# Performance work log

Hardware: AMD Instinct MI355X
Metric: run time of the kernel (lower is better)

Reference implementation:

```python
import jax, jax.numpy as jnp
import numpy as np

N, E, IN, H = 10000, 320000, 128, 64

def setup_inputs() -> dict:
    key = jax.random.key(0)
    ks = jax.random.split(key, 6)
    x = jax.random.normal(ks[0], (N, IN), dtype=jnp.float32)
    edge_index = jax.random.randint(ks[1], (2, E), 0, N)
    edge_weight = jax.random.uniform(ks[2], (E,), dtype=jnp.float32)
    W_rel = jax.random.normal(ks[3], (IN, H), dtype=jnp.float32) / np.float32(np.sqrt(IN))
    W_root = jax.random.normal(ks[4], (IN, H), dtype=jnp.float32) / np.float32(np.sqrt(IN))
    b = jnp.zeros((H,), dtype=jnp.float32)
    return {"x": x, "edge_index": edge_index, "edge_weight": edge_weight,
            "W_rel": W_rel, "W_root": W_root, "b": b}

def reference(x, edge_index, edge_weight, W_rel, W_root, b):
    # GraphConv (PyG): out_i = W_rel @ sum_{j->i} e_ji * x_j + W_root @ x_i + b
    src, dst = edge_index[0], edge_index[1]
    msgs = x[src] * edge_weight[:, None]                    # [E, IN] gather
    agg = jax.ops.segment_sum(msgs, dst, num_segments=N)    # [N, IN] scatter-add
    z = agg @ W_rel + x @ W_root + b                        # [N, H]
    # (activation=None, dropout inactive in eval, no BN)
    adj = jax.nn.sigmoid(z @ z.T)                           # [N, N] inner-product decoder
    return adj, z
```

## Files before the change

kernel.cpp:

```cpp
#include <hip/hip_runtime.h>
#include <hip/hip_bf16.h>
#include <stdint.h>

#define N_NODES 10000
#define N_EDGES 320000
#define DIM_IN  128
#define DIM_H   64
#define SSTR    72

typedef __attribute__((ext_vector_type(8))) short  short8;
typedef __attribute__((ext_vector_type(4))) float  f32x4;

__device__ __forceinline__ unsigned short f2bf(float f) {
    union { float f; unsigned int i; } v; v.f = f;
    unsigned int u = v.i;
    return (unsigned short)((u + 0x7fffu + ((u >> 16) & 1u)) >> 16);
}

__global__ void hist_kernel(const int* __restrict__ ei, int* __restrict__ deg) {
    int e = blockIdx.x * blockDim.x + threadIdx.x;
    if (e < N_EDGES) atomicAdd(&deg[ei[N_EDGES + e]], 1);
}

__global__ void __launch_bounds__(1024) scan_kernel(const int* __restrict__ deg,
                                                    int* __restrict__ offs,
                                                    int* __restrict__ cursor) {
    __shared__ int part[1024];
    int t = threadIdx.x;
    int base = t * 10;
    int local[10];
    int s = 0;
    for (int i = 0; i < 10; ++i) {
        int idx = base + i;
        int d = (idx < N_NODES) ? deg[idx] : 0;
        local[i] = d; s += d;
    }
    part[t] = s;
    __syncthreads();
    for (int o = 1; o < 1024; o <<= 1) {
        int add = (t >= o) ? part[t - o] : 0;
        __syncthreads();
        part[t] += add;
        __syncthreads();
    }
    int run = part[t] - s;
    for (int i = 0; i < 10; ++i) {
        int idx = base + i;
        if (idx < N_NODES) { offs[idx] = run; cursor[idx] = run; run += local[i]; }
    }
    if (t == 1023) offs[N_NODES] = part[1023];
}

__global__ void bucket_kernel(const int* __restrict__ ei, int* __restrict__ cursor,
                              int* __restrict__ esorted) {
    int e = blockIdx.x * blockDim.x + threadIdx.x;
    if (e < N_EDGES) {
        int d = ei[N_EDGES + e];
        int slot = atomicAdd(&cursor[d], 1);
        esorted[slot] = e;
    }
}

__global__ void __launch_bounds__(64) agg_dense_kernel(
    const float* __restrict__ x,
    const int* __restrict__ ei,
    const float* __restrict__ ew,
    const float* __restrict__ wrel,
    const float* __restrict__ wroot,
    const float* __restrict__ bias,
    const int* __restrict__ offs,
    const int* __restrict__ esorted,
    float* __restrict__ out)
{
    int i = blockIdx.x;
    int lane = threadIdx.x;
    __shared__ float aggL[DIM_IN];
    __shared__ float xL[DIM_IN];

    int beg = offs[i], end = offs[i + 1];
    const float2* xrow_i = (const float2*)(x + (size_t)i * DIM_IN);
    float2 xi = xrow_i[lane];
    float a0 = 0.f, a1 = 0.f;
    for (int p = beg; p < end; ++p) {
        int e = esorted[p];
        int s = ei[e];
        float w = ew[e];
        float2 xv = ((const float2*)(x + (size_t)s * DIM_IN))[lane];
        a0 += w * xv.x;
        a1 += w * xv.y;
    }
    aggL[2 * lane]     = a0;
    aggL[2 * lane + 1] = a1;
    xL[2 * lane]       = xi.x;
    xL[2 * lane + 1]   = xi.y;
    __syncthreads();

    int h = lane;
    float acc = bias[h];
    for (int k = 0; k < DIM_IN; ++k) {
        acc += aggL[k] * wrel[k * DIM_H + h];
        acc += xL[k]   * wroot[k * DIM_H + h];
    }
    out[(size_t)N_NODES * N_NODES + (size_t)i * DIM_H + h] = acc;
}

__global__ void __launch_bounds__(256) gemm_sig_kernel(float* __restrict__ out)
{
    const float* zf = out + (size_t)N_NODES * N_NODES;
    __shared__ unsigned short sA[128 * SSTR];
    __shared__ unsigned short sB[128 * SSTR];

    int t    = threadIdx.x;
    int lane = t & 63;
    int wave = t >> 6;
    int wm = wave >> 1, wn = wave & 1;
    int i0 = blockIdx.x * 128;
    int j0 = blockIdx.y * 128;
    int l15  = lane & 15;
    int quad = lane >> 4;

    {
        int r  = t >> 4;
        int c4 = (t & 15) << 2;
        #pragma unroll
        for (int pass = 0; pass < 8; ++pass) {
            int row = pass * 16 + r;
            int ga = i0 + row; if (ga >= N_NODES) ga = N_NODES - 1;
            int gb = j0 + row; if (gb >= N_NODES) gb = N_NODES - 1;
            float4 va = *(const float4*)(zf + (size_t)ga * DIM_H + c4);
            float4 vb = *(const float4*)(zf + (size_t)gb * DIM_H + c4);
            ushort4 ha, hb;
            ha.x = f2bf(va.x); ha.y = f2bf(va.y); ha.z = f2bf(va.z); ha.w = f2bf(va.w);
            hb.x = f2bf(vb.x); hb.y = f2bf(vb.y); hb.z = f2bf(vb.z); hb.w = f2bf(vb.w);
            *(ushort4*)(&sA[row * SSTR + c4]) = ha;
            *(ushort4*)(&sB[row * SSTR + c4]) = hb;
        }
    }
    __syncthreads();

    f32x4 acc[4][4];
    #pragma unroll
    for (int a = 0; a < 4; ++a)
        #pragma unroll
        for (int b = 0; b < 4; ++b) acc[a][b] = (f32x4)0.f;

    #pragma unroll
    for (int s = 0; s < 2; ++s) {
        int kb = quad * 8 + s * 32;
        short8 af[4], bfr[4];
        #pragma unroll
        for (int mi = 0; mi < 4; ++mi)
            af[mi] = *(const short8*)(&sA[(wm * 64 + mi * 16 + l15) * SSTR + kb]);
        #pragma unroll
        for (int ni = 0; ni < 4; ++ni)
            bfr[ni] = *(const short8*)(&sB[(wn * 64 + ni * 16 + l15) * SSTR + kb]);
        #pragma unroll
        for (int mi = 0; mi < 4; ++mi)
            #pragma unroll
            for (int ni = 0; ni < 4; ++ni)
                acc[mi][ni] = __builtin_amdgcn_mfma_f32_16x16x32_bf16(
                    af[mi], bfr[ni], acc[mi][ni], 0, 0, 0);
    }

    bool full = (i0 + 127 < N_NODES) && (j0 + 127 < N_NODES);
    if (full) {
        #pragma unroll
        for (int mi = 0; mi < 4; ++mi) {
            #pragma unroll
            for (int ni = 0; ni < 4; ++ni) {
                int col = j0 + wn * 64 + ni * 16 + l15;
                #pragma unroll
                for (int r = 0; r < 4; ++r) {
                    int row = i0 + wm * 64 + mi * 16 + quad * 4 + r;
                    float v  = acc[mi][ni][r];
                    float sg = 1.0f / (1.0f + __expf(-v));
                    out[(size_t)row * N_NODES + col] = sg;
                }
            }
        }
    } else {
        #pragma unroll
        for (int mi = 0; mi < 4; ++mi) {
            #pragma unroll
            for (int ni = 0; ni < 4; ++ni) {
                int col = j0 + wn * 64 + ni * 16 + l15;
                #pragma unroll
                for (int r = 0; r < 4; ++r) {
                    int row = i0 + wm * 64 + mi * 16 + quad * 4 + r;
                    if (row < N_NODES && col < N_NODES) {
                        float v  = acc[mi][ni][r];
                        float sg = 1.0f / (1.0f + __expf(-v));
                        out[(size_t)row * N_NODES + col] = sg;
                    }
                }
            }
        }
    }
}

extern "C" void kernel_launch(void* const* d_in, const int* in_sizes, int n_in,
                              void* d_out, int out_size, void* d_ws, size_t ws_size,
                              hipStream_t stream) {
    const float* x     = (const float*)d_in[0];
    const int*   ei    = (const int*)d_in[1];
    const float* ew    = (const float*)d_in[2];
    const float* wrel  = (const float*)d_in[3];
    const float* wroot = (const float*)d_in[4];
    const float* bias  = (const float*)d_in[5];
    float* out = (float*)d_out;

    char* base = (char*)d_out;
    int* esorted = (int*)(base);
    int* deg     = (int*)(base + 1280000);
    int* offs    = (int*)(base + 1320000);
    int* cursor  = (int*)(base + 1360004);

    hipMemsetAsync(deg, 0, N_NODES * sizeof(int), stream);
    hist_kernel<<<(N_EDGES + 255) / 256, 256, 0, stream>>>(ei, deg);
    scan_kernel<<<1, 1024, 0, stream>>>(deg, offs, cursor);
    bucket_kernel<<<(N_EDGES + 255) / 256, 256, 0, stream>>>(ei, cursor, esorted);
    agg_dense_kernel<<<N_NODES, 64, 0, stream>>>(x, ei, ew, wrel, wroot, bias,
                                                 offs, esorted, out);
    dim3 grid((N_NODES + 127) / 128, (N_NODES + 127) / 128);
    gemm_sig_kernel<<<grid, 256, 0, stream>>>(out);
}
```

Measured before the change: 566.9 us.

## Stage GEMM output tile through LDS for coalesced nontemporal float4 stores

```diff
diff --git a/kernel.cpp b/kernel.cpp
--- a/kernel.cpp
+++ b/kernel.cpp
@@ -7,6 +7,7 @@
 #define DIM_IN  128
 #define DIM_H   64
 #define SSTR    72
+#define CSTR    132
 
 typedef __attribute__((ext_vector_type(8))) short  short8;
 typedef __attribute__((ext_vector_type(4))) float  f32x4;
@@ -107,15 +108,16 @@
 __global__ void __launch_bounds__(256) gemm_sig_kernel(float* __restrict__ out)
 {
     const float* zf = out + (size_t)N_NODES * N_NODES;
-    __shared__ unsigned short sA[128 * SSTR];
-    __shared__ unsigned short sB[128 * SSTR];
+    __shared__ __align__(16) unsigned short sAB[2 * 128 * SSTR];
+    unsigned short* sA = sAB;
+    unsigned short* sB = sAB + 128 * SSTR;
 
     int t    = threadIdx.x;
     int lane = t & 63;
     int wave = t >> 6;
     int wm = wave >> 1, wn = wave & 1;
-    int i0 = blockIdx.x * 128;
-    int j0 = blockIdx.y * 128;
+    int j0 = blockIdx.x * 128;
+    int i0 = blockIdx.y * 128;
     int l15  = lane & 15;
     int quad = lane >> 4;
 
@@ -162,37 +164,38 @@
                     af[mi], bfr[ni], acc[mi][ni], 0, 0, 0);
     }
 
-    bool full = (i0 + 127 < N_NODES) && (j0 + 127 < N_NODES);
-    if (full) {
-        #pragma unroll
-        for (int mi = 0; mi < 4; ++mi) {
+    float* sC = (float*)sAB;
+    #pragma unroll
+    for (int half = 0; half < 2; ++half) {
+        __syncthreads();
+        if (wm == half) {
             #pragma unroll
-            for (int ni = 0; ni < 4; ++ni) {
-                int col = j0 + wn * 64 + ni * 16 + l15;
+            for (int mi = 0; mi < 4; ++mi)
                 #pragma unroll
-                for (int r = 0; r < 4; ++r) {
-                    int row = i0 + wm * 64 + mi * 16 + quad * 4 + r;
-                    float v  = acc[mi][ni][r];
-                    float sg = 1.0f / (1.0f + __expf(-v));
-                    out[(size_t)row * N_NODES + col] = sg;
-                }
-            }
+                for (int ni = 0; ni < 4; ++ni)
+                    #pragma unroll
+                    for (int r = 0; r < 4; ++r)
+                        sC[(mi * 16 + quad * 4 + r) * CSTR + wn * 64 + ni * 16 + l15]
+                            = acc[mi][ni][r];
         }
-    } else {
-        #pragma unroll
-        for (int mi = 0; mi < 4; ++mi) {
-            #pragma unroll
-            for (int ni = 0; ni < 4; ++ni) {
-                int col = j0 + wn * 64 + ni * 16 + l15;
-                #pragma unroll
-                for (int r = 0; r < 4; ++r) {
-                    int row = i0 + wm * 64 + mi * 16 + quad * 4 + r;
-                    if (row < N_NODES && col < N_NODES) {
-                        float v  = acc[mi][ni][r];
-                        float sg = 1.0f / (1.0f + __expf(-v));
-                        out[(size_t)row * N_NODES + col] = sg;
-                    }
-                }
+        __syncthreads();
+        int i0h = i0 + half * 64;
+        #pragma unroll
+        for (int it = 0; it < 8; ++it) {
+            int idx = it * 256 + t;
+            int row = idx >> 5;
+            int c4  = (idx & 31) << 2;
+            f32x4 v = *(const f32x4*)&sC[row * CSTR + c4];
+            f32x4 sg;
+            sg.x = 1.0f / (1.0f + __expf(-v.x));
+            sg.y = 1.0f / (1.0f + __expf(-v.y));
+            sg.z = 1.0f / (1.0f + __expf(-v.z));
+            sg.w = 1.0f / (1.0f + __expf(-v.w));
+            int grow = i0h + row;
+            int gcol = j0 + c4;
+            if (grow < N_NODES && gcol + 3 < N_NODES) {
+                __builtin_nontemporal_store(
+                    sg, (f32x4*)(out + (size_t)grow * N_NODES + gcol));
             }
         }
     }
```

Measured after the change: 521.2 us. -8.1%, faster.
